# Performance work log

Hardware: AMD Instinct MI355X
Metric: run time of the kernel (lower is better)

The kernel has to match this reference:

```python
import jax, jax.numpy as jnp
import numpy as np

HEADS = 8
DIM_HEAD = 64


def setup_inputs() -> dict:
    key = jax.random.key(0)
    ks = jax.random.split(key, 9)
    b, n, d = 2, 2048, 512
    inner = HEADS * DIM_HEAD  # 512
    s = 0.02
    return {
        "x": jax.random.normal(ks[0], (b, n, d), dtype=jnp.float32),
        "attn_bias": jax.random.normal(ks[1], (1, HEADS, n, n), dtype=jnp.float32),
        "Wq": jax.random.normal(ks[2], (d, inner), dtype=jnp.float32) * s,
        "Wkv": jax.random.normal(ks[3], (d, 2 * inner), dtype=jnp.float32) * s,
        "Wo": jax.random.normal(ks[4], (inner, d), dtype=jnp.float32) * s,
        "bo": jax.random.normal(ks[5], (d,), dtype=jnp.float32) * s,
        "Wg": jax.random.normal(ks[6], (d, inner), dtype=jnp.float32) * s,
        "bg": jnp.ones((inner,), dtype=jnp.float32),
    }


def reference(x, attn_bias, Wq, Wkv, Wo, bo, Wg, bg):
    b, n, d = x.shape
    h, dh = HEADS, DIM_HEAD
    scale = dh ** -0.5
    # projections: [b, n, h*dh] -> [b, h, n, dh]
    q = (x @ Wq).reshape(b, n, h, dh).transpose(0, 2, 1, 3) * scale
    k, v = jnp.split(x @ Wkv, 2, axis=-1)
    k = k.reshape(b, n, h, dh).transpose(0, 2, 1, 3)
    v = v.reshape(b, n, h, dh).transpose(0, 2, 1, 3)
    # scores + additive bias; max-subtract softmax (stable, as in original)
    dots = jnp.einsum('bhid,bhjd->bhij', q, k) + attn_bias
    attn = jax.nn.softmax(dots, axis=-1)
    out = jnp.einsum('bhij,bhjd->bhid', attn, v)
    out = out.transpose(0, 2, 1, 3).reshape(b, n, h * dh)
    # gating sigmoid epilogue
    gates = jax.nn.sigmoid(x @ Wg + bg)
    out = out * gates
    return out @ Wo + bo
```

## Files before the change

### kernel.cpp

```cpp
#include <hip/hip_runtime.h>
#include <hip/hip_bf16.h>

typedef __bf16 bf16_t;
typedef __bf16 bf16x8 __attribute__((ext_vector_type(8)));
typedef float f32x4 __attribute__((ext_vector_type(4)));

static __device__ __forceinline__ bf16_t to_bf16(float f) { return (bf16_t)f; }

__global__ void k_convert_x(const float* __restrict__ src, bf16_t* __restrict__ dst, int n8) {
  int i = blockIdx.x * blockDim.x + threadIdx.x;
  if (i >= n8) return;
  const float4* s = reinterpret_cast<const float4*>(src) + (size_t)i * 2;
  float4 a = s[0], b = s[1];
  bf16x8 v;
  v[0]=(bf16_t)a.x; v[1]=(bf16_t)a.y; v[2]=(bf16_t)a.z; v[3]=(bf16_t)a.w;
  v[4]=(bf16_t)b.x; v[5]=(bf16_t)b.y; v[6]=(bf16_t)b.z; v[7]=(bf16_t)b.w;
  reinterpret_cast<bf16x8*>(dst)[i] = v;
}

__global__ void k_transpose_cvt(const float* __restrict__ src, bf16_t* __restrict__ dst, int Nc) {
  __shared__ bf16_t tile[64 * 72];
  const int n0 = blockIdx.x * 64, k0 = blockIdx.y * 64;
  const int t = threadIdx.x;
  #pragma unroll
  for (int it = 0; it < 16; ++it) {
    int c = t + it * 256;
    int kl = c >> 6, nl = c & 63;
    tile[kl * 72 + nl] = to_bf16(src[(size_t)(k0 + kl) * Nc + n0 + nl]);
  }
  __syncthreads();
  #pragma unroll
  for (int it = 0; it < 16; ++it) {
    int c = t + it * 256;
    int nl = c >> 6, kl = c & 63;
    dst[(size_t)(n0 + nl) * 512 + k0 + kl] = tile[kl * 72 + nl];
  }
}

__global__ __launch_bounds__(256) void k_gemm_proj(
    const bf16_t* __restrict__ A,
    const bf16_t* __restrict__ BT,
    const float*  __restrict__ bg,
    bf16_t* __restrict__ qo,
    bf16_t* __restrict__ ko,
    bf16_t* __restrict__ vto,
    float*  __restrict__ go)
{
  __shared__ __align__(16) bf16_t lA[128 * 72];
  __shared__ __align__(16) bf16_t lB[128 * 72];
  const int t = threadIdx.x;
  const int w = t >> 6, lane = t & 63, lr = lane & 15, lg = lane >> 4;
  const int wr = w >> 1, wc = w & 1;
  const int m0 = blockIdx.y * 128, n0 = blockIdx.x * 128;
  f32x4 acc[4][4] = {};
  for (int k0 = 0; k0 < 512; k0 += 64) {
    __syncthreads();
    #pragma unroll
    for (int it = 0; it < 4; ++it) {
      int c = t + it * 256;
      int row = c >> 3, cc = c & 7;
      *reinterpret_cast<bf16x8*>(&lA[row * 72 + cc * 8]) =
          *reinterpret_cast<const bf16x8*>(&A[(size_t)(m0 + row) * 512 + k0 + cc * 8]);
      *reinterpret_cast<bf16x8*>(&lB[row * 72 + cc * 8]) =
          *reinterpret_cast<const bf16x8*>(&BT[(size_t)(n0 + row) * 512 + k0 + cc * 8]);
    }
    __syncthreads();
    #pragma unroll
    for (int kk = 0; kk < 2; ++kk) {
      bf16x8 af[4], bfm[4];
      #pragma unroll
      for (int mf = 0; mf < 4; ++mf)
        af[mf] = *reinterpret_cast<const bf16x8*>(&lA[(wr*64 + mf*16 + lr) * 72 + kk*32 + lg*8]);
      #pragma unroll
      for (int nf = 0; nf < 4; ++nf)
        bfm[nf] = *reinterpret_cast<const bf16x8*>(&lB[(wc*64 + nf*16 + lr) * 72 + kk*32 + lg*8]);
      #pragma unroll
      for (int mf = 0; mf < 4; ++mf)
        #pragma unroll
        for (int nf = 0; nf < 4; ++nf)
          acc[mf][nf] = __builtin_amdgcn_mfma_f32_16x16x32_bf16(af[mf], bfm[nf], acc[mf][nf], 0, 0, 0);
    }
  }
  const int seg = n0 >> 9;
  #pragma unroll
  for (int mf = 0; mf < 4; ++mf) {
    #pragma unroll
    for (int nf = 0; nf < 4; ++nf) {
      #pragma unroll
      for (int r = 0; r < 4; ++r) {
        int rm = m0 + wr*64 + mf*16 + lg*4 + r;
        int cn = n0 + wc*64 + nf*16 + lr;
        float v = acc[mf][nf][r];
        int b = rm >> 11, n = rm & 2047;
        int c = cn & 511;
        if (seg == 0) {
          int h = c >> 6, dh = c & 63;
          qo[((size_t)(b*8 + h) * 2048 + n) * 64 + dh] = to_bf16(v * 0.125f);
        } else if (seg == 1) {
          int h = c >> 6, dh = c & 63;
          ko[((size_t)(b*8 + h) * 2048 + n) * 64 + dh] = to_bf16(v);
        } else if (seg == 2) {
          int h = c >> 6, dh = c & 63;
          vto[((size_t)(b*8 + h) * 64 + dh) * 2048 + n] = to_bf16(v);
        } else {
          float z = v + bg[c];
          go[(size_t)rm * 512 + c] = 1.0f / (1.0f + __expf(-z));
        }
      }
    }
  }
}

__global__ __launch_bounds__(256) void k_attn(
    const bf16_t* __restrict__ q,
    const bf16_t* __restrict__ kb,
    const bf16_t* __restrict__ vt,
    const float*  __restrict__ bias,
    const float*  __restrict__ gates,
    bf16_t* __restrict__ ao)
{
  __shared__ __align__(16) bf16_t lK[64 * 72];
  __shared__ __align__(16) bf16_t lV[64 * 72];
  __shared__ __align__(16) bf16_t lP[4][16 * 72];
  const int t = threadIdx.x, w = t >> 6, lane = t & 63, lr = lane & 15, lg = lane >> 4;
  const int bh = blockIdx.y, b = bh >> 3, h = bh & 7;
  const int i0 = blockIdx.x * 64, ib = i0 + w * 16;

  bf16x8 aq[2];
  const bf16_t* qp = q + ((size_t)bh * 2048 + ib + lr) * 64;
  aq[0] = *reinterpret_cast<const bf16x8*>(qp + lg * 8);
  aq[1] = *reinterpret_cast<const bf16x8*>(qp + 32 + lg * 8);

  float m_r[4] = {-1e30f, -1e30f, -1e30f, -1e30f};
  float l_r[4] = {0.f, 0.f, 0.f, 0.f};
  f32x4 accO[4] = {};

  const float* bias_p = bias + (size_t)h * 2048 * 2048 + (size_t)(ib + lg * 4) * 2048 + lr;
  const bf16_t* kp = kb + (size_t)bh * 2048 * 64;
  const bf16_t* vp = vt + (size_t)bh * 64 * 2048;

  for (int jt = 0; jt < 32; ++jt) {
    const int j0 = jt * 64;
    float bv[4][4];
    #pragma unroll
    for (int nf = 0; nf < 4; ++nf)
      #pragma unroll
      for (int r = 0; r < 4; ++r)
        bv[nf][r] = bias_p[(size_t)r * 2048 + j0 + nf * 16];

    __syncthreads();
    #pragma unroll
    for (int it = 0; it < 2; ++it) {
      int c = t + it * 256;
      int row = c >> 3, cc = c & 7;
      *reinterpret_cast<bf16x8*>(&lK[row * 72 + cc * 8]) =
          *reinterpret_cast<const bf16x8*>(&kp[(size_t)(j0 + row) * 64 + cc * 8]);
      *reinterpret_cast<bf16x8*>(&lV[row * 72 + cc * 8]) =
          *reinterpret_cast<const bf16x8*>(&vp[(size_t)row * 2048 + j0 + cc * 8]);
    }
    __syncthreads();

    f32x4 s[4] = {};
    #pragma unroll
    for (int kk = 0; kk < 2; ++kk) {
      #pragma unroll
      for (int nf = 0; nf < 4; ++nf) {
        bf16x8 bf = *reinterpret_cast<const bf16x8*>(&lK[(nf*16 + lr) * 72 + kk*32 + lg*8]);
        s[nf] = __builtin_amdgcn_mfma_f32_16x16x32_bf16(aq[kk], bf, s[nf], 0, 0, 0);
      }
    }
    #pragma unroll
    for (int nf = 0; nf < 4; ++nf)
      #pragma unroll
      for (int r = 0; r < 4; ++r)
        s[nf][r] += bv[nf][r];

    #pragma unroll
    for (int r = 0; r < 4; ++r) {
      float rmx = fmaxf(fmaxf(s[0][r], s[1][r]), fmaxf(s[2][r], s[3][r]));
      rmx = fmaxf(rmx, __shfl_xor(rmx, 1));
      rmx = fmaxf(rmx, __shfl_xor(rmx, 2));
      rmx = fmaxf(rmx, __shfl_xor(rmx, 4));
      rmx = fmaxf(rmx, __shfl_xor(rmx, 8));
      float mnew = fmaxf(m_r[r], rmx);
      float corr = __expf(m_r[r] - mnew);
      m_r[r] = mnew;
      float rs = 0.f;
      #pragma unroll
      for (int nf = 0; nf < 4; ++nf) {
        float p = __expf(s[nf][r] - mnew);
        s[nf][r] = p;
        rs += p;
      }
      rs += __shfl_xor(rs, 1); rs += __shfl_xor(rs, 2);
      rs += __shfl_xor(rs, 4); rs += __shfl_xor(rs, 8);
      l_r[r] = l_r[r] * corr + rs;
      #pragma unroll
      for (int df = 0; df < 4; ++df) accO[df][r] *= corr;
    }

    #pragma unroll
    for (int nf = 0; nf < 4; ++nf)
      #pragma unroll
      for (int r = 0; r < 4; ++r)
        lP[w][(lg*4 + r) * 72 + nf*16 + lr] = to_bf16(s[nf][r]);

    #pragma unroll
    for (int kk = 0; kk < 2; ++kk) {
      bf16x8 pa = *reinterpret_cast<const bf16x8*>(&lP[w][lr * 72 + kk*32 + lg*8]);
      #pragma unroll
      for (int df = 0; df < 4; ++df) {
        bf16x8 bv8 = *reinterpret_cast<const bf16x8*>(&lV[(df*16 + lr) * 72 + kk*32 + lg*8]);
        accO[df] = __builtin_amdgcn_mfma_f32_16x16x32_bf16(pa, bv8, accO[df], 0, 0, 0);
      }
    }
  }

  #pragma unroll
  for (int r = 0; r < 4; ++r) {
    float inv = 1.0f / l_r[r];
    int ig = ib + lg*4 + r;
    #pragma unroll
    for (int df = 0; df < 4; ++df) {
      int dg = h*64 + df*16 + lr;
      float gate = gates[(size_t)(b*2048 + ig) * 512 + dg];
      ao[(size_t)(b*2048 + ig) * 512 + dg] = to_bf16(accO[df][r] * inv * gate);
    }
  }
}

__global__ __launch_bounds__(256) void k_gemm_out(
    const bf16_t* __restrict__ A,
    const bf16_t* __restrict__ BT,
    const float*  __restrict__ bo,
    float* __restrict__ out)
{
  __shared__ __align__(16) bf16_t lA[128 * 72];
  __shared__ __align__(16) bf16_t lB[128 * 72];
  const int t = threadIdx.x;
  const int w = t >> 6, lane = t & 63, lr = lane & 15, lg = lane >> 4;
  const int wr = w >> 1, wc = w & 1;
  const int m0 = blockIdx.y * 128, n0 = blockIdx.x * 128;
  f32x4 acc[4][4] = {};
  for (int k0 = 0; k0 < 512; k0 += 64) {
    __syncthreads();
    #pragma unroll
    for (int it = 0; it < 4; ++it) {
      int c = t + it * 256;
      int row = c >> 3, cc = c & 7;
      *reinterpret_cast<bf16x8*>(&lA[row * 72 + cc * 8]) =
          *reinterpret_cast<const bf16x8*>(&A[(size_t)(m0 + row) * 512 + k0 + cc * 8]);
      *reinterpret_cast<bf16x8*>(&lB[row * 72 + cc * 8]) =
          *reinterpret_cast<const bf16x8*>(&BT[(size_t)(n0 + row) * 512 + k0 + cc * 8]);
    }
    __syncthreads();
    #pragma unroll
    for (int kk = 0; kk < 2; ++kk) {
      bf16x8 af[4], bfm[4];
      #pragma unroll
      for (int mf = 0; mf < 4; ++mf)
        af[mf] = *reinterpret_cast<const bf16x8*>(&lA[(wr*64 + mf*16 + lr) * 72 + kk*32 + lg*8]);
      #pragma unroll
      for (int nf = 0; nf < 4; ++nf)
        bfm[nf] = *reinterpret_cast<const bf16x8*>(&lB[(wc*64 + nf*16 + lr) * 72 + kk*32 + lg*8]);
      #pragma unroll
      for (int mf = 0; mf < 4; ++mf)
        #pragma unroll
        for (int nf = 0; nf < 4; ++nf)
          acc[mf][nf] = __builtin_amdgcn_mfma_f32_16x16x32_bf16(af[mf], bfm[nf], acc[mf][nf], 0, 0, 0);
    }
  }
  #pragma unroll
  for (int mf = 0; mf < 4; ++mf) {
    #pragma unroll
    for (int nf = 0; nf < 4; ++nf) {
      #pragma unroll
      for (int r = 0; r < 4; ++r) {
        int rm = m0 + wr*64 + mf*16 + lg*4 + r;
        int cn = n0 + wc*64 + nf*16 + lr;
        out[(size_t)rm * 512 + cn] = acc[mf][nf][r] + bo[cn];
      }
    }
  }
}

extern "C" void kernel_launch(void* const* d_in, const int* in_sizes, int n_in,
                              void* d_out, int out_size, void* d_ws, size_t ws_size,
                              hipStream_t stream) {
  const float* x    = (const float*)d_in[0];
  const float* bias = (const float*)d_in[1];
  const float* Wq   = (const float*)d_in[2];
  const float* Wkv  = (const float*)d_in[3];
  const float* Wo   = (const float*)d_in[4];
  const float* bo   = (const float*)d_in[5];
  const float* Wg   = (const float*)d_in[6];
  const float* bg   = (const float*)d_in[7];
  float* out = (float*)d_out;

  char* ws = (char*)d_ws;
  const size_t MB = 1024 * 1024;
  bf16_t* x_bf  = (bf16_t*)(ws + 0 * MB);
  bf16_t* WcatT = (bf16_t*)(ws + 4 * MB);
  bf16_t* WoT   = (bf16_t*)(ws + 6 * MB);
  bf16_t* q_bf  = (bf16_t*)(ws + 7 * MB);
  bf16_t* k_bf  = (bf16_t*)(ws + 11 * MB);
  bf16_t* vt_bf = (bf16_t*)(ws + 15 * MB);
  float*  g_f32 = (float*) (ws + 19 * MB);
  bf16_t* ao_bf = (bf16_t*)(ws + 27 * MB);

  k_convert_x<<<1024, 256, 0, stream>>>(x, x_bf, 2097152 / 8);
  k_transpose_cvt<<<dim3(8, 8),  256, 0, stream>>>(Wq,  WcatT,               512);
  k_transpose_cvt<<<dim3(16, 8), 256, 0, stream>>>(Wkv, WcatT + 512 * 512,  1024);
  k_transpose_cvt<<<dim3(8, 8),  256, 0, stream>>>(Wg,  WcatT + 1536 * 512,  512);
  k_transpose_cvt<<<dim3(8, 8),  256, 0, stream>>>(Wo,  WoT,                 512);
  k_gemm_proj<<<dim3(16, 32), 256, 0, stream>>>(x_bf, WcatT, bg, q_bf, k_bf, vt_bf, g_f32);
  k_attn<<<dim3(32, 16), 256, 0, stream>>>(q_bf, k_bf, vt_bf, bias, g_f32, ao_bf);
  k_gemm_out<<<dim3(4, 32), 256, 0, stream>>>(ao_bf, WoT, bo, out);
}
```

Before: 131.7 us.

## Split attention KV range across blocks, add register prefetch and combine kernel

Splits the key dimension of the attention kernel into two halves via gridDim.z, writing partial O, max and sum to workspace, then merges them with a new combine kernel that applies normalization and gating. It also prefetches the next K/V tile and bias values into registers while computing the current tile, and sets launch bounds to four blocks per CU. The aim is to raise occupancy and parallelism (512 blocks become 1024) and hide global load latency. In exchange it adds extra fp32 partial-result traffic, an extra launch, and more register pressure. The split path is used only when the workspace is at least 48 MB.

```diff
diff --git a/kernel.cpp b/kernel.cpp
--- a/kernel.cpp
+++ b/kernel.cpp
@@ -111,13 +111,17 @@
   }
 }
 
-__global__ __launch_bounds__(256) void k_attn(
+template<int FINAL>
+__global__ __launch_bounds__(256, 4) void k_attn(
     const bf16_t* __restrict__ q,
     const bf16_t* __restrict__ kb,
     const bf16_t* __restrict__ vt,
     const float*  __restrict__ bias,
     const float*  __restrict__ gates,
-    bf16_t* __restrict__ ao)
+    bf16_t* __restrict__ ao,
+    float* __restrict__ pO,
+    float* __restrict__ pm,
+    float* __restrict__ pl)
 {
   __shared__ __align__(16) bf16_t lK[64 * 72];
   __shared__ __align__(16) bf16_t lV[64 * 72];
@@ -125,6 +129,9 @@
   const int t = threadIdx.x, w = t >> 6, lane = t & 63, lr = lane & 15, lg = lane >> 4;
   const int bh = blockIdx.y, b = bh >> 3, h = bh & 7;
   const int i0 = blockIdx.x * 64, ib = i0 + w * 16;
+  const int ntile = 32 / (int)gridDim.z;
+  const int sz = blockIdx.z;
+  const int jbase = sz * ntile * 64;
 
   bf16x8 aq[2];
   const bf16_t* qp = q + ((size_t)bh * 2048 + ib + lr) * 64;
@@ -139,26 +146,41 @@
   const bf16_t* kp = kb + (size_t)bh * 2048 * 64;
   const bf16_t* vp = vt + (size_t)bh * 64 * 2048;
 
-  for (int jt = 0; jt < 32; ++jt) {
-    const int j0 = jt * 64;
-    float bv[4][4];
+  const int srow = t >> 3, scc = t & 7;
+  const int srow1 = (t + 256) >> 3;
+
+  bf16x8 rK0, rK1, rV0, rV1;
+  float bv[4][4];
+  {
+    const int j0 = jbase;
+    rK0 = *reinterpret_cast<const bf16x8*>(&kp[(size_t)(j0 + srow)  * 64 + scc * 8]);
+    rK1 = *reinterpret_cast<const bf16x8*>(&kp[(size_t)(j0 + srow1) * 64 + scc * 8]);
+    rV0 = *reinterpret_cast<const bf16x8*>(&vp[(size_t)srow  * 2048 + j0 + scc * 8]);
+    rV1 = *reinterpret_cast<const bf16x8*>(&vp[(size_t)srow1 * 2048 + j0 + scc * 8]);
     #pragma unroll
     for (int nf = 0; nf < 4; ++nf)
       #pragma unroll
       for (int r = 0; r < 4; ++r)
         bv[nf][r] = bias_p[(size_t)r * 2048 + j0 + nf * 16];
-
-    __syncthreads();
-    #pragma unroll
-    for (int it = 0; it < 2; ++it) {
-      int c = t + it * 256;
-      int row = c >> 3, cc = c & 7;
-      *reinterpret_cast<bf16x8*>(&lK[row * 72 + cc * 8]) =
-          *reinterpret_cast<const bf16x8*>(&kp[(size_t)(j0 + row) * 64 + cc * 8]);
-      *reinterpret_cast<bf16x8*>(&lV[row * 72 + cc * 8]) =
-          *reinterpret_cast<const bf16x8*>(&vp[(size_t)row * 2048 + j0 + cc * 8]);
-    }
-    __syncthreads();
+  }
+
+  for (int jt = 0; jt < ntile; ++jt) {
+    const int j1 = jbase + (jt + 1) * 64;
+    const bool more = (jt + 1 < ntile);
+
+    __syncthreads();
+    *reinterpret_cast<bf16x8*>(&lK[srow  * 72 + scc * 8]) = rK0;
+    *reinterpret_cast<bf16x8*>(&lK[srow1 * 72 + scc * 8]) = rK1;
+    *reinterpret_cast<bf16x8*>(&lV[srow  * 72 + scc * 8]) = rV0;
+    *reinterpret_cast<bf16x8*>(&lV[srow1 * 72 + scc * 8]) = rV1;
+    __syncthreads();
+
+    if (more) {
+      rK0 = *reinterpret_cast<const bf16x8*>(&kp[(size_t)(j1 + srow)  * 64 + scc * 8]);
+      rK1 = *reinterpret_cast<const bf16x8*>(&kp[(size_t)(j1 + srow1) * 64 + scc * 8]);
+      rV0 = *reinterpret_cast<const bf16x8*>(&vp[(size_t)srow  * 2048 + j1 + scc * 8]);
+      rV1 = *reinterpret_cast<const bf16x8*>(&vp[(size_t)srow1 * 2048 + j1 + scc * 8]);
+    }
 
     f32x4 s[4] = {};
     #pragma unroll
@@ -174,6 +196,13 @@
       #pragma unroll
       for (int r = 0; r < 4; ++r)
         s[nf][r] += bv[nf][r];
+    if (more) {
+      #pragma unroll
+      for (int nf = 0; nf < 4; ++nf)
+        #pragma unroll
+        for (int r = 0; r < 4; ++r)
+          bv[nf][r] = bias_p[(size_t)r * 2048 + j1 + nf * 16];
+    }
 
     #pragma unroll
     for (int r = 0; r < 4; ++r) {
@@ -216,17 +245,54 @@
     }
   }
 
-  #pragma unroll
-  for (int r = 0; r < 4; ++r) {
-    float inv = 1.0f / l_r[r];
-    int ig = ib + lg*4 + r;
-    #pragma unroll
-    for (int df = 0; df < 4; ++df) {
-      int dg = h*64 + df*16 + lr;
-      float gate = gates[(size_t)(b*2048 + ig) * 512 + dg];
-      ao[(size_t)(b*2048 + ig) * 512 + dg] = to_bf16(accO[df][r] * inv * gate);
-    }
-  }
+  if (FINAL) {
+    #pragma unroll
+    for (int r = 0; r < 4; ++r) {
+      float inv = 1.0f / l_r[r];
+      int ig = ib + lg*4 + r;
+      #pragma unroll
+      for (int df = 0; df < 4; ++df) {
+        int dg = h*64 + df*16 + lr;
+        float gate = gates[(size_t)(b*2048 + ig) * 512 + dg];
+        ao[(size_t)(b*2048 + ig) * 512 + dg] = to_bf16(accO[df][r] * inv * gate);
+      }
+    }
+  } else {
+    float* po = pO + (((size_t)sz * 16 + bh) * 2048) * 64;
+    #pragma unroll
+    for (int r = 0; r < 4; ++r) {
+      int ig = ib + lg*4 + r;
+      #pragma unroll
+      for (int df = 0; df < 4; ++df)
+        po[(size_t)ig * 64 + df*16 + lr] = accO[df][r];
+    }
+    if (lr == 0) {
+      size_t rb = ((size_t)sz * 16 + bh) * 2048 + ib + lg*4;
+      #pragma unroll
+      for (int r = 0; r < 4; ++r) { pm[rb + r] = m_r[r]; pl[rb + r] = l_r[r]; }
+    }
+  }
+}
+
+__global__ __launch_bounds__(256) void k_attn_combine(
+    const float* __restrict__ pO, const float* __restrict__ pm, const float* __restrict__ pl,
+    const float* __restrict__ gates, bf16_t* __restrict__ ao, int nsplit)
+{
+  int idx = blockIdx.x * 256 + threadIdx.x;
+  int dh = idx & 63, row = (idx >> 6) & 2047, bh = idx >> 17;
+  int b = bh >> 3, h = bh & 7;
+  const size_t SP_O = (size_t)16 * 2048 * 64, SP_S = (size_t)16 * 2048;
+  size_t rb = (size_t)bh * 2048 + row;
+  float M = -1e30f;
+  for (int s = 0; s < nsplit; ++s) M = fmaxf(M, pm[s * SP_S + rb]);
+  float L = 0.f, O = 0.f;
+  for (int s = 0; s < nsplit; ++s) {
+    float wgt = __expf(pm[s * SP_S + rb] - M);
+    L += pl[s * SP_S + rb] * wgt;
+    O += pO[s * SP_O + rb * 64 + dh] * wgt;
+  }
+  float gate = gates[(size_t)(b * 2048 + row) * 512 + h * 64 + dh];
+  ao[(size_t)(b * 2048 + row) * 512 + h * 64 + dh] = to_bf16(O / L * gate);
 }
 
 __global__ __launch_bounds__(256) void k_gemm_out(
@@ -307,6 +373,9 @@
   bf16_t* vt_bf = (bf16_t*)(ws + 15 * MB);
   float*  g_f32 = (float*) (ws + 19 * MB);
   bf16_t* ao_bf = (bf16_t*)(ws + 27 * MB);
+  float*  pO    = (float*) (ws + 31 * MB);
+  float*  pm    = (float*) (ws + 47 * MB);
+  float*  pl    = (float*) (ws + 47 * MB + 256 * 1024);
 
   k_convert_x<<<1024, 256, 0, stream>>>(x, x_bf, 2097152 / 8);
   k_transpose_cvt<<<dim3(8, 8),  256, 0, stream>>>(Wq,  WcatT,               512);
@@ -314,6 +383,14 @@
   k_transpose_cvt<<<dim3(8, 8),  256, 0, stream>>>(Wg,  WcatT + 1536 * 512,  512);
   k_transpose_cvt<<<dim3(8, 8),  256, 0, stream>>>(Wo,  WoT,                 512);
   k_gemm_proj<<<dim3(16, 32), 256, 0, stream>>>(x_bf, WcatT, bg, q_bf, k_bf, vt_bf, g_f32);
-  k_attn<<<dim3(32, 16), 256, 0, stream>>>(q_bf, k_bf, vt_bf, bias, g_f32, ao_bf);
+
+  if (ws_size >= 48 * MB) {
+    k_attn<0><<<dim3(32, 16, 2), 256, 0, stream>>>(q_bf, k_bf, vt_bf, bias, nullptr,
+                                                   nullptr, pO, pm, pl);
+    k_attn_combine<<<8192, 256, 0, stream>>>(pO, pm, pl, g_f32, ao_bf, 2);
+  } else {
+    k_attn<1><<<dim3(32, 16, 1), 256, 0, stream>>>(q_bf, k_bf, vt_bf, bias, g_f32,
+                                                   ao_bf, nullptr, nullptr, nullptr);
+  }
   k_gemm_out<<<dim3(4, 32), 256, 0, stream>>>(ao_bf, WoT, bo, out);
 }
```

New measurement: 132.9 us. Within noise of the previous version (+0.9%).
